# Optimization experiments

Measured on AMD Instinct MI355X. Metric: run time of the kernel, lower is better.

## Reference

```python
import jax, jax.numpy as jnp
import numpy as np

D_MODEL, D_FFN, N_LEVELS, N_HEADS, N_POINTS = 256, 1024, 4, 8, 4
B, LQ = 2, 8192
SHAPES = [(128, 128), (64, 64), (32, 32), (16, 16)]  # (H_l, W_l) per level
D_HEAD = D_MODEL // N_HEADS


def setup_inputs() -> dict:
    key = jax.random.key(0)
    ks = jax.random.split(key, 16)
    S = sum(h * w for h, w in SHAPES)

    def lin_w(k, fin, fout):
        s = 1.0 / np.sqrt(fin)
        return jax.random.uniform(k, (fin, fout), jnp.float32, -s, s)

    inp = {
        "tgt": jax.random.normal(ks[0], (B, LQ, D_MODEL), jnp.float32),
        "query_pos": jax.random.normal(ks[1], (B, LQ, D_MODEL), jnp.float32),
        "reference_points": jax.random.uniform(ks[2], (B, LQ, N_LEVELS, 2), jnp.float32),
        "src": jax.random.normal(ks[3], (B, S, D_MODEL), jnp.float32),
        "spatial_shapes": np.array(SHAPES, dtype=np.int64),
        "level_start_index": np.concatenate([[0], np.cumsum([h * w for h, w in SHAPES])[:-1]]).astype(np.int64),
        "W_value": lin_w(ks[4], D_MODEL, D_MODEL),
        "b_value": jnp.zeros((D_MODEL,), jnp.float32),
        "W_off": lin_w(ks[5], D_MODEL, N_HEADS * N_LEVELS * N_POINTS * 2),
        "b_off": 0.5 * jax.random.normal(ks[6], (N_HEADS * N_LEVELS * N_POINTS * 2,), jnp.float32),
        "W_attn": lin_w(ks[7], D_MODEL, N_HEADS * N_LEVELS * N_POINTS),
        "b_attn": jnp.zeros((N_HEADS * N_LEVELS * N_POINTS,), jnp.float32),
        "W_out": lin_w(ks[8], D_MODEL, D_MODEL),
        "b_out": jnp.zeros((D_MODEL,), jnp.float32),
        "ln1_g": jnp.ones((D_MODEL,), jnp.float32),
        "ln1_b": jnp.zeros((D_MODEL,), jnp.float32),
        "W1": lin_w(ks[9], D_MODEL, D_FFN),
        "b1": jnp.zeros((D_FFN,), jnp.float32),
        "W2": lin_w(ks[10], D_FFN, D_MODEL),
        "b2": jnp.zeros((D_MODEL,), jnp.float32),
        "ln3_g": jnp.ones((D_MODEL,), jnp.float32),
        "ln3_b": jnp.zeros((D_MODEL,), jnp.float32),
    }
    return inp


def _layer_norm(x, g, b, eps=1e-5):
    mu = jnp.mean(x, -1, keepdims=True)
    var = jnp.mean((x - mu) ** 2, -1, keepdims=True)
    return (x - mu) * jax.lax.rsqrt(var + eps) * g + b


def _ms_deform_attn(q, reference_points, src, shapes,
                    W_value, b_value, W_off, b_off, W_attn, b_attn, W_out, b_out):
    Bq, Lq, _ = q.shape
    value = (src @ W_value + b_value).reshape(Bq, -1, N_HEADS, D_HEAD)
    value = jnp.transpose(value, (0, 2, 1, 3))  # [B, H, S, Dh]
    off = (q @ W_off + b_off).reshape(Bq, Lq, N_HEADS, N_LEVELS, N_POINTS, 2)
    attn = jax.nn.softmax((q @ W_attn + b_attn).reshape(Bq, Lq, N_HEADS, N_LEVELS * N_POINTS), axis=-1)
    attn = attn.reshape(Bq, Lq, N_HEADS, N_LEVELS, N_POINTS)
    # offset normalizer is (W_l, H_l) per level
    normalizer = jnp.array([[w, h] for h, w in shapes], jnp.float32)
    loc = reference_points[:, :, None, :, None, :] + off / normalizer[None, None, None, :, None, :]

    out = jnp.zeros((Bq, Lq, N_HEADS, D_HEAD), jnp.float32)
    start = 0
    for l, (Hl, Wl) in enumerate(shapes):
        Nl = Hl * Wl
        v_l = value[:, :, start:start + Nl]  # [B, H, Nl, Dh]
        start += Nl
        loc_l = jnp.transpose(loc[:, :, :, l, :, :], (0, 2, 1, 3, 4))  # [B, H, Lq, P, 2]
        # grid_sample (align_corners=False, zero padding) pixel coords
        x = loc_l[..., 0] * Wl - 0.5
        y = loc_l[..., 1] * Hl - 0.5
        x0, y0 = jnp.floor(x), jnp.floor(y)
        wx, wy = x - x0, y - y0
        acc = jnp.zeros((Bq, N_HEADS, Lq, N_POINTS, D_HEAD), jnp.float32)
        for dx, dy, w in ((0, 0, (1 - wx) * (1 - wy)), (1, 0, wx * (1 - wy)),
                          (0, 1, (1 - wx) * wy), (1, 1, wx * wy)):
            xi, yi = x0 + dx, y0 + dy
            valid = (xi >= 0) & (xi < Wl) & (yi >= 0) & (yi < Hl)
            idx = (jnp.clip(yi, 0, Hl - 1) * Wl + jnp.clip(xi, 0, Wl - 1)).astype(jnp.int32)
            g = jnp.take_along_axis(v_l, idx.reshape(Bq, N_HEADS, -1, 1), axis=2)
            g = g.reshape(Bq, N_HEADS, Lq, N_POINTS, D_HEAD)
            acc = acc + jnp.where(valid[..., None], w[..., None] * g, 0.0)
        a = jnp.transpose(attn[:, :, :, l, :], (0, 2, 1, 3))  # [B, H, Lq, P]
        out = out + jnp.einsum('bhqp,bhqpd->bqhd', a, acc)
    return out.reshape(Bq, Lq, D_MODEL) @ W_out + b_out


def reference(tgt, query_pos, reference_points, src, spatial_shapes, level_start_index,
              W_value, b_value, W_off, b_off, W_attn, b_attn, W_out, b_out,
              ln1_g, ln1_b, W1, b1, W2, b2, ln3_g, ln3_b):
    shapes = [(int(h), int(w)) for h, w in np.asarray(spatial_shapes)]
    q = tgt + query_pos  # with_pos_embed
    tgt2 = _ms_deform_attn(q, reference_points, src, shapes,
                           W_value, b_value, W_off, b_off, W_attn, b_attn, W_out, b_out)
    x = _layer_norm(tgt + tgt2, ln1_g, ln1_b)  # dropout = identity (eval)
    ff = jax.nn.relu(x @ W1 + b1) @ W2 + b2
    return _layer_norm(x + ff, ln3_g, ln3_b)
```

## Files before the change

### kernel.cpp

```cpp
#include <hip/hip_runtime.h>
#include <hip/hip_bf16.h>
#include <math.h>

#define D_MODEL   256
#define D_FFN     1024
#define N_LEVELS  4
#define N_HEADS   8
#define N_POINTS  4
#define BATCH     2
#define LQ        8192
#define S_TOTAL   21760
#define M_Q       (BATCH*LQ)
#define M_V       (BATCH*S_TOTAL)
#define VTILES    (M_V/128)

typedef __attribute__((ext_vector_type(8))) short bf16x8;
typedef __attribute__((ext_vector_type(4))) float floatx4;

struct alignas(8)  bh4 { __hip_bfloat16 a, b, c, d; };
struct alignas(16) bh8 { __hip_bfloat16 v[8]; };

__device__ __forceinline__ void gld_lds16(const void* g, void* l) {
    __builtin_amdgcn_global_load_lds(
        (const __attribute__((address_space(1))) void*)g,
        (__attribute__((address_space(3))) void*)l, 16, 0, 0);
}

template<int BM, int BN, int K>
__device__ __forceinline__ void gemm_core(const __hip_bfloat16* __restrict__ A,
                                          const __hip_bfloat16* __restrict__ Bt,
                                          int row0, int nb0,
                                          short* As, short* Bs,
                                          floatx4 (&acc)[BM/64][BN/16])
{
    constexpr int NT  = BN / 16;
    constexpr int AF  = BM / 64;
    constexpr int BCH = BN / 64;
    constexpr int NIT = K / 32;

    const int tid  = threadIdx.x;
    const int w    = tid >> 6;
    const int lane = tid & 63;
    const int quad = lane >> 4;
    const int l15  = lane & 15;
    const size_t K2 = (size_t)K * 2;

    const char* gA[AF]; int lA[AF];
#pragma unroll
    for (int i = 0; i < AF; i++) {
        int o = (w * AF + i) * 1024 + lane * 16;
        gA[i] = (const char*)A + (size_t)(row0 + (o >> 6)) * K2 + (o & 63);
        lA[i] = (w * AF + i) * 512;
    }
    const char* gB[BCH]; int lB[BCH];
#pragma unroll
    for (int j = 0; j < BCH; j++) {
        int o = (w * BCH + j) * 1024 + lane * 16;
        gB[j] = (const char*)Bt + (size_t)(nb0 + (o >> 6)) * K2 + (o & 63);
        lB[j] = (w * BCH + j) * 512;
    }

#pragma unroll
    for (int i = 0; i < AF; i++)  gld_lds16(gA[i], &As[lA[i]]);
#pragma unroll
    for (int j = 0; j < BCH; j++) gld_lds16(gB[j], &Bs[lB[j]]);

#pragma unroll 8
    for (int it = 0; it < NIT; ++it) {
        __syncthreads();
        const int cb = it & 1;
        if (it + 1 < NIT) {
            const size_t kb = (size_t)(it + 1) * 64;
            const int nb = cb ^ 1;
#pragma unroll
            for (int i = 0; i < AF; i++)  gld_lds16(gA[i] + kb, &As[nb * BM * 32 + lA[i]]);
#pragma unroll
            for (int j = 0; j < BCH; j++) gld_lds16(gB[j] + kb, &Bs[nb * BN * 32 + lB[j]]);
        }
        const short* Ab = &As[cb * BM * 32];
        const short* Bb = &Bs[cb * BN * 32];
        bf16x8 af[AF];
#pragma unroll
        for (int mi = 0; mi < AF; mi++)
            af[mi] = *(const bf16x8*)&Ab[(w * (AF * 16) + mi * 16 + l15) * 32 + quad * 8];
#pragma unroll
        for (int ni = 0; ni < NT; ni++) {
            bf16x8 bfr = *(const bf16x8*)&Bb[(ni * 16 + l15) * 32 + quad * 8];
#pragma unroll
            for (int mi = 0; mi < AF; mi++)
                acc[mi][ni] = __builtin_amdgcn_mfma_f32_16x16x32_bf16(af[mi], bfr, acc[mi][ni], 0, 0, 0);
        }
    }
}

template<int BM, int BN, int K, int EPI>
__global__ __launch_bounds__(256)
void mfma_gemm(const __hip_bfloat16* __restrict__ A,
               const __hip_bfloat16* __restrict__ Bt,
               const float* __restrict__ bias,
               const float* __restrict__ resid,
               const float* __restrict__ lng, const float* __restrict__ lnb,
               float* __restrict__ outf, __hip_bfloat16* __restrict__ outb,
               int ldOut)
{
    constexpr int NT = BN / 16, AF = BM / 64;
    __shared__ alignas(16) short As[2 * BM * 32];
    __shared__ alignas(16) short Bs[2 * BN * 32];

    const int tid = threadIdx.x, w = tid >> 6, lane = tid & 63;
    const int quad = lane >> 4, l15 = lane & 15;
    const int row0 = blockIdx.x * BM, nb0 = blockIdx.y * BN;

    floatx4 acc[AF][NT];
#pragma unroll
    for (int mi = 0; mi < AF; mi++)
#pragma unroll
        for (int ni = 0; ni < NT; ni++) acc[mi][ni] = (floatx4){0.f, 0.f, 0.f, 0.f};

    gemm_core<BM, BN, K>(A, Bt, row0, nb0, As, Bs, acc);

    float bias_c[NT];
#pragma unroll
    for (int ni = 0; ni < NT; ni++) bias_c[ni] = bias[nb0 + ni * 16 + l15];

    if (EPI == 4) {
        float gv[NT], bv[NT];
#pragma unroll
        for (int ni = 0; ni < NT; ni++) { gv[ni] = lng[ni * 16 + l15]; bv[ni] = lnb[ni * 16 + l15]; }
#pragma unroll
        for (int mi = 0; mi < AF; mi++)
#pragma unroll
            for (int r = 0; r < 4; r++) {
                int row = row0 + w * (AF * 16) + mi * 16 + quad * 4 + r;
                size_t rb = (size_t)row * 256;
                float s = 0.f, sq = 0.f, vv[NT];
#pragma unroll
                for (int ni = 0; ni < NT; ni++) {
                    float v = acc[mi][ni][r] + bias_c[ni] + resid[rb + ni * 16 + l15];
                    vv[ni] = v; s += v; sq += v * v;
                }
#pragma unroll
                for (int msk = 1; msk <= 8; msk <<= 1) {
                    s += __shfl_xor(s, msk); sq += __shfl_xor(sq, msk);
                }
                float mean = s * (1.f / 256.f);
                float var  = sq * (1.f / 256.f) - mean * mean;
                float rstd = rsqrtf(var + 1e-5f);
#pragma unroll
                for (int ni = 0; ni < NT; ni++) {
                    float o = (vv[ni] - mean) * rstd * gv[ni] + bv[ni];
                    outf[rb + ni * 16 + l15] = o;
                    if (outb) outb[rb + ni * 16 + l15] = __float2bfloat16(o);
                }
            }
        return;
    }

#pragma unroll
    for (int mi = 0; mi < AF; mi++)
#pragma unroll
        for (int r = 0; r < 4; r++) {
            int row = row0 + w * (AF * 16) + mi * 16 + quad * 4 + r;
            size_t rb = (size_t)row * ldOut + nb0;
#pragma unroll
            for (int ni = 0; ni < NT; ni++) {
                float v = fmaxf(acc[mi][ni][r] + bias_c[ni], 0.f);
                outb[rb + ni * 16 + l15] = __float2bfloat16(v);
            }
        }
}

__global__ __launch_bounds__(256)
void mfma_gemm_vq(const __hip_bfloat16* __restrict__ srcb,
                  const __hip_bfloat16* __restrict__ Wvt,
                  const float* __restrict__ b_value,
                  __hip_bfloat16* __restrict__ valueb,
                  const __hip_bfloat16* __restrict__ qb,
                  const __hip_bfloat16* __restrict__ Woat,
                  const float* __restrict__ b_off, const float* __restrict__ b_attn,
                  float* __restrict__ offb, float* __restrict__ attnb)
{
    __shared__ alignas(16) short As[2 * 128 * 32];
    __shared__ alignas(16) short Bs[2 * 128 * 32];

    const bool isV = blockIdx.x < VTILES;
    if (isV && blockIdx.y == 2) return;

    const int tid = threadIdx.x, w = tid >> 6, lane = tid & 63;
    const int quad = lane >> 4, l15 = lane & 15;
    const int nb0 = blockIdx.y * 128;

    floatx4 acc[2][8];
#pragma unroll
    for (int mi = 0; mi < 2; mi++)
#pragma unroll
        for (int ni = 0; ni < 8; ni++) acc[mi][ni] = (floatx4){0.f, 0.f, 0.f, 0.f};

    if (isV) {
        const int row0 = blockIdx.x * 128;
        gemm_core<128, 128, 256>(srcb, Wvt, row0, nb0, As, Bs, acc);
        float bias_c[8];
#pragma unroll
        for (int ni = 0; ni < 8; ni++) bias_c[ni] = b_value[nb0 + ni * 16 + l15];
#pragma unroll
        for (int mi = 0; mi < 2; mi++)
#pragma unroll
            for (int r = 0; r < 4; r++) {
                int row = row0 + w * 32 + mi * 16 + quad * 4 + r;
                size_t rb = (size_t)row * 256 + nb0;
#pragma unroll
                for (int ni = 0; ni < 8; ni++)
                    valueb[rb + ni * 16 + l15] = __float2bfloat16(acc[mi][ni][r] + bias_c[ni]);
            }
        return;
    }

    const int row0 = (blockIdx.x - VTILES) * 128;
    gemm_core<128, 128, 256>(qb, Woat, row0, nb0, As, Bs, acc);

    if (blockIdx.y < 2) {
        float bias_c[8];
#pragma unroll
        for (int ni = 0; ni < 8; ni++) bias_c[ni] = b_off[nb0 + ni * 16 + l15];
#pragma unroll
        for (int mi = 0; mi < 2; mi++)
#pragma unroll
            for (int r = 0; r < 4; r++) {
                int row = row0 + w * 32 + mi * 16 + quad * 4 + r;
                size_t rb = (size_t)row * 256 + nb0;
#pragma unroll
                for (int ni = 0; ni < 8; ni++)
                    offb[rb + ni * 16 + l15] = acc[mi][ni][r] + bias_c[ni];
            }
    } else {
        float bias_c[8];
#pragma unroll
        for (int ni = 0; ni < 8; ni++) bias_c[ni] = b_attn[ni * 16 + l15];
#pragma unroll
        for (int mi = 0; mi < 2; mi++)
#pragma unroll
            for (int r = 0; r < 4; r++) {
                int row = row0 + w * 32 + mi * 16 + quad * 4 + r;
                size_t rb = (size_t)row * 128;
#pragma unroll
                for (int ni = 0; ni < 8; ni++) {
                    float v = acc[mi][ni][r] + bias_c[ni];
                    float m = v;
#pragma unroll
                    for (int msk = 1; msk <= 8; msk <<= 1) m = fmaxf(m, __shfl_xor(m, msk));
                    float e = __expf(v - m);
                    float ssum = e;
#pragma unroll
                    for (int msk = 1; msk <= 8; msk <<= 1) ssum += __shfl_xor(ssum, msk);
                    attnb[rb + ni * 16 + l15] = e / ssum;
                }
            }
    }
}

__global__ __launch_bounds__(256)
void prep_kernel(const float* w0, const float* w1, const float* w2,
                 const float* w3, const float* w4, const float* w5,
                 __hip_bfloat16* o0, __hip_bfloat16* o1, __hip_bfloat16* o2,
                 __hip_bfloat16* o3, __hip_bfloat16* o4, __hip_bfloat16* o5,
                 const float* src, __hip_bfloat16* srcb,
                 const float* tgt, const float* qpos, __hip_bfloat16* qb)
{
    const int bx = blockIdx.x;
    if (bx < 736) {
        int t = bx;
        const float* s; __hip_bfloat16* dst; int Kd, Nd, tl;
        if      (t < 64)  { s = w0; dst = o0; Kd = 256;  Nd = 256;  tl = t; }
        else if (t < 128) { s = w1; dst = o1; Kd = 256;  Nd = 256;  tl = t - 64; }
        else if (t < 160) { s = w2; dst = o2; Kd = 256;  Nd = 128;  tl = t - 128; }
        else if (t < 224) { s = w3; dst = o3; Kd = 256;  Nd = 256;  tl = t - 160; }
        else if (t < 480) { s = w4; dst = o4; Kd = 256;  Nd = 1024; tl = t - 224; }
        else              { s = w5; dst = o5; Kd = 1024; Nd = 256;  tl = t - 480; }
        int ntn = Nd >> 5;
        int kt = tl / ntn, nt = tl - kt * ntn;
        __shared__ float T[32][33];
        int tx = threadIdx.x & 31, ty = threadIdx.x >> 5;
#pragma unroll
        for (int i = 0; i < 4; i++) {
            int k = kt * 32 + ty + i * 8;
            T[tx][ty + i * 8] = s[(size_t)k * Nd + nt * 32 + tx];
        }
        __syncthreads();
#pragma unroll
        for (int i = 0; i < 4; i++) {
            int n = nt * 32 + ty + i * 8;
            dst[(size_t)n * Kd + kt * 32 + tx] = __float2bfloat16(T[ty + i * 8][tx]);
        }
    } else if (bx < 736 + 10880) {
        int i = (bx - 736) * 256 + threadIdx.x;
        float4 v = ((const float4*)src)[i];
        ((bh4*)srcb)[i] = { __float2bfloat16(v.x), __float2bfloat16(v.y),
                            __float2bfloat16(v.z), __float2bfloat16(v.w) };
    } else {
        int i = (bx - 736 - 10880) * 256 + threadIdx.x;
        float4 x = ((const float4*)tgt)[i];
        float4 y = ((const float4*)qpos)[i];
        ((bh4*)qb)[i] = { __float2bfloat16(x.x + y.x), __float2bfloat16(x.y + y.y),
                          __float2bfloat16(x.z + y.z), __float2bfloat16(x.w + y.w) };
    }
}

#define QB 8
__global__ __launch_bounds__(256)
void sample_kernel(const float* __restrict__ refp, const float* __restrict__ offb,
                   const float* __restrict__ attn,
                   const __hip_bfloat16* __restrict__ value,
                   __hip_bfloat16* __restrict__ tgt2)
{
    __shared__ int2 spk[64 * 65];

    const int q0  = blockIdx.x * QB;
    const int tid = threadIdx.x;

#pragma unroll
    for (int k = 0; k < 4; k++) {
        const int it = tid + k * 256;
        const int ql = it >> 7, h = (it >> 4) & 7, lp = it & 15;
        const int l = lp >> 2, p = lp & 3;
        const int q = q0 + ql, b = q >> 13;
        const int Wl = 128 >> l;
        const int LST = (l == 0) ? 0 : (l == 1) ? 16384 : (l == 2) ? 20480 : 21504;

        const float rx = refp[((size_t)q * N_LEVELS + l) * 2 + 0];
        const float ry = refp[((size_t)q * N_LEVELS + l) * 2 + 1];
        const float ox = offb[(size_t)q * 256 + h * 32 + l * 8 + p * 2 + 0];
        const float oy = offb[(size_t)q * 256 + h * 32 + l * 8 + p * 2 + 1];
        const float a  = attn[(size_t)q * 128 + h * 16 + lp];

        const float x = rx * Wl - 0.5f + ox;
        const float y = ry * Wl - 0.5f + oy;
        const float x0f = floorf(x), y0f = floorf(y);
        const float wx = x - x0f, wy = y - y0f;
        const int ix = (int)x0f, iy = (int)y0f;
        const int base = b * S_TOTAL + LST;
        const int g = ql * 8 + h;
        const float cw[4] = {(1.f - wx) * (1.f - wy) * a, wx * (1.f - wy) * a,
                             (1.f - wx) * wy * a,         wx * wy * a};
#pragma unroll
        for (int c = 0; c < 4; c++) {
            const int xi = ix + (c & 1), yi = iy + (c >> 1);
            const bool valid = ((unsigned)xi < (unsigned)Wl) && ((unsigned)yi < (unsigned)Wl);
            spk[(lp * 4 + c) * 65 + g] =
                make_int2(valid ? base + yi * Wl + xi : base,
                          __float_as_int(valid ? cw[c] : 0.f));
        }
    }
    __syncthreads();

    const int ql = tid >> 5, h = (tid >> 2) & 7, d4 = tid & 3;
    const int q = q0 + ql, g = ql * 8 + h;
    const int c0 = h * 32 + d4 * 8;
    const char* vb = (const char*)value + (size_t)c0 * 2;

    float ac[8] = {0.f, 0.f, 0.f, 0.f, 0.f, 0.f, 0.f, 0.f};
#pragma unroll
    for (int sc = 0; sc < 64; sc++) {
        int2 pk = spk[sc * 65 + g];
        float wv = __int_as_float(pk.y);
        uint4 rv = *(const uint4*)(vb + ((size_t)(unsigned)pk.x << 9));
        ac[0] += wv * __uint_as_float(rv.x << 16);
        ac[1] += wv * __uint_as_float(rv.x & 0xffff0000u);
        ac[2] += wv * __uint_as_float(rv.y << 16);
        ac[3] += wv * __uint_as_float(rv.y & 0xffff0000u);
        ac[4] += wv * __uint_as_float(rv.z << 16);
        ac[5] += wv * __uint_as_float(rv.z & 0xffff0000u);
        ac[6] += wv * __uint_as_float(rv.w << 16);
        ac[7] += wv * __uint_as_float(rv.w & 0xffff0000u);
    }
    bh8 o;
#pragma unroll
    for (int i = 0; i < 8; i++) o.v[i] = __float2bfloat16(ac[i]);
    *(bh8*)(tgt2 + (size_t)q * 256 + c0) = o;
}

extern "C" void kernel_launch(void* const* d_in, const int* in_sizes, int n_in,
                              void* d_out, int out_size, void* d_ws, size_t ws_size,
                              hipStream_t stream) {
    const float* tgt     = (const float*)d_in[0];
    const float* qpos    = (const float*)d_in[1];
    const float* refp    = (const float*)d_in[2];
    const float* src     = (const float*)d_in[3];
    const float* W_value = (const float*)d_in[6];
    const float* b_value = (const float*)d_in[7];
    const float* W_off   = (const float*)d_in[8];
    const float* b_off   = (const float*)d_in[9];
    const float* W_attn  = (const float*)d_in[10];
    const float* b_attn  = (const float*)d_in[11];
    const float* W_out   = (const float*)d_in[12];
    const float* b_out   = (const float*)d_in[13];
    const float* ln1_g   = (const float*)d_in[14];
    const float* ln1_b   = (const float*)d_in[15];
    const float* W1      = (const float*)d_in[16];
    const float* b1      = (const float*)d_in[17];
    const float* W2      = (const float*)d_in[18];
    const float* b2      = (const float*)d_in[19];
    const float* ln3_g   = (const float*)d_in[20];
    const float* ln3_b   = (const float*)d_in[21];
    float* out = (float*)d_out;

    char* p = (char*)d_ws;
    auto nxt = [&](size_t b) { char* r = p; p += (b + 255) & ~(size_t)255; return r; };
    __hip_bfloat16* Wvt    = (__hip_bfloat16*)nxt((size_t)256 * 256 * 2);
    __hip_bfloat16* Woat   = (__hip_bfloat16*)nxt((size_t)384 * 256 * 2);
    __hip_bfloat16* Woutt  = (__hip_bfloat16*)nxt((size_t)256 * 256 * 2);
    __hip_bfloat16* W1t    = (__hip_bfloat16*)nxt((size_t)1024 * 256 * 2);
    __hip_bfloat16* W2t    = (__hip_bfloat16*)nxt((size_t)256 * 1024 * 2);
    __hip_bfloat16* srcb   = (__hip_bfloat16*)nxt((size_t)M_V * 256 * 2);
    __hip_bfloat16* qb     = (__hip_bfloat16*)nxt((size_t)M_Q * 256 * 2);
    __hip_bfloat16* valueb = (__hip_bfloat16*)nxt((size_t)M_V * 256 * 2);
    float*          offb   = (float*)nxt((size_t)M_Q * 256 * 4);
    float*          attnb  = (float*)nxt((size_t)M_Q * 128 * 4);
    __hip_bfloat16* tgt2b  = (__hip_bfloat16*)nxt((size_t)M_Q * 256 * 2);
    float*          x      = (float*)nxt((size_t)M_Q * 256 * 4);
    __hip_bfloat16* xb     = (__hip_bfloat16*)nxt((size_t)M_Q * 256 * 2);
    __hip_bfloat16* hb     = (__hip_bfloat16*)nxt((size_t)M_Q * 1024 * 2);

    dim3 blk(256);

    prep_kernel<<<dim3(736 + 10880 + 4096), blk, 0, stream>>>(
        W_value, W_off, W_attn, W_out, W1, W2,
        Wvt, Woat, Woat + 256 * 256, Woutt, W1t, W2t,
        src, srcb, tgt, qpos, qb);

    mfma_gemm_vq<<<dim3(VTILES + M_Q / 128, 3), blk, 0, stream>>>(
        srcb, Wvt, b_value, valueb, qb, Woat, b_off, b_attn, offb, attnb);

    sample_kernel<<<dim3(M_Q / QB), blk, 0, stream>>>(refp, offb, attnb, valueb, tgt2b);

    mfma_gemm<64, 256, 256, 4><<<dim3(M_Q / 64, 1), blk, 0, stream>>>(
        tgt2b, Woutt, b_out, tgt, ln1_g, ln1_b, x, xb, 256);

    mfma_gemm<128, 128, 256, 2><<<dim3(M_Q / 128, 8), blk, 0, stream>>>(
        xb, W1t, b1, nullptr, nullptr, nullptr, nullptr, hb, 1024);

    mfma_gemm<64, 256, 1024, 4><<<dim3(M_Q / 64, 1), blk, 0, stream>>>(
        hb, W2t, b2, x, ln3_g, ln3_b, out, nullptr, 256);
}
```

Measured before the change: 306.8 us.

## Split GEMM epilogue LayerNorm into separate kernels, split-K FFN2, pack sample metadata

```diff
diff --git a/kernel.cpp b/kernel.cpp
--- a/kernel.cpp
+++ b/kernel.cpp
@@ -1,5 +1,6 @@
 #include <hip/hip_runtime.h>
 #include <hip/hip_bf16.h>
+#include <hip/hip_fp16.h>
 #include <math.h>
 
 #define D_MODEL   256
@@ -29,7 +30,7 @@
 template<int BM, int BN, int K>
 __device__ __forceinline__ void gemm_core(const __hip_bfloat16* __restrict__ A,
                                           const __hip_bfloat16* __restrict__ Bt,
-                                          int row0, int nb0,
+                                          int row0, int nb0, int lda, int ldb,
                                           short* As, short* Bs,
                                           floatx4 (&acc)[BM/64][BN/16])
 {
@@ -43,20 +44,20 @@
     const int lane = tid & 63;
     const int quad = lane >> 4;
     const int l15  = lane & 15;
-    const size_t K2 = (size_t)K * 2;
+    const size_t ldaB = (size_t)lda * 2, ldbB = (size_t)ldb * 2;
 
     const char* gA[AF]; int lA[AF];
 #pragma unroll
     for (int i = 0; i < AF; i++) {
         int o = (w * AF + i) * 1024 + lane * 16;
-        gA[i] = (const char*)A + (size_t)(row0 + (o >> 6)) * K2 + (o & 63);
+        gA[i] = (const char*)A + (size_t)(row0 + (o >> 6)) * ldaB + (o & 63);
         lA[i] = (w * AF + i) * 512;
     }
     const char* gB[BCH]; int lB[BCH];
 #pragma unroll
     for (int j = 0; j < BCH; j++) {
         int o = (w * BCH + j) * 1024 + lane * 16;
-        gB[j] = (const char*)Bt + (size_t)(nb0 + (o >> 6)) * K2 + (o & 63);
+        gB[j] = (const char*)Bt + (size_t)(nb0 + (o >> 6)) * ldbB + (o & 63);
         lB[j] = (w * BCH + j) * 512;
     }
 
@@ -98,10 +99,8 @@
 void mfma_gemm(const __hip_bfloat16* __restrict__ A,
                const __hip_bfloat16* __restrict__ Bt,
                const float* __restrict__ bias,
-               const float* __restrict__ resid,
-               const float* __restrict__ lng, const float* __restrict__ lnb,
                float* __restrict__ outf, __hip_bfloat16* __restrict__ outb,
-               int ldOut)
+               int lda, int ldb, int ldOut, long zStride)
 {
     constexpr int NT = BN / 16, AF = BM / 64;
     __shared__ alignas(16) short As[2 * BM * 32];
@@ -110,6 +109,7 @@
     const int tid = threadIdx.x, w = tid >> 6, lane = tid & 63;
     const int quad = lane >> 4, l15 = lane & 15;
     const int row0 = blockIdx.x * BM, nb0 = blockIdx.y * BN;
+    const int z = blockIdx.z;
 
     floatx4 acc[AF][NT];
 #pragma unroll
@@ -117,45 +117,14 @@
 #pragma unroll
         for (int ni = 0; ni < NT; ni++) acc[mi][ni] = (floatx4){0.f, 0.f, 0.f, 0.f};
 
-    gemm_core<BM, BN, K>(A, Bt, row0, nb0, As, Bs, acc);
+    gemm_core<BM, BN, K>(A + (size_t)z * K, Bt + (size_t)z * K,
+                         row0, nb0, lda, ldb, As, Bs, acc);
 
     float bias_c[NT];
 #pragma unroll
-    for (int ni = 0; ni < NT; ni++) bias_c[ni] = bias[nb0 + ni * 16 + l15];
-
-    if (EPI == 4) {
-        float gv[NT], bv[NT];
-#pragma unroll
-        for (int ni = 0; ni < NT; ni++) { gv[ni] = lng[ni * 16 + l15]; bv[ni] = lnb[ni * 16 + l15]; }
-#pragma unroll
-        for (int mi = 0; mi < AF; mi++)
-#pragma unroll
-            for (int r = 0; r < 4; r++) {
-                int row = row0 + w * (AF * 16) + mi * 16 + quad * 4 + r;
-                size_t rb = (size_t)row * 256;
-                float s = 0.f, sq = 0.f, vv[NT];
-#pragma unroll
-                for (int ni = 0; ni < NT; ni++) {
-                    float v = acc[mi][ni][r] + bias_c[ni] + resid[rb + ni * 16 + l15];
-                    vv[ni] = v; s += v; sq += v * v;
-                }
-#pragma unroll
-                for (int msk = 1; msk <= 8; msk <<= 1) {
-                    s += __shfl_xor(s, msk); sq += __shfl_xor(sq, msk);
-                }
-                float mean = s * (1.f / 256.f);
-                float var  = sq * (1.f / 256.f) - mean * mean;
-                float rstd = rsqrtf(var + 1e-5f);
-#pragma unroll
-                for (int ni = 0; ni < NT; ni++) {
-                    float o = (vv[ni] - mean) * rstd * gv[ni] + bv[ni];
-                    outf[rb + ni * 16 + l15] = o;
-                    if (outb) outb[rb + ni * 16 + l15] = __float2bfloat16(o);
-                }
-            }
-        return;
-    }
-
+    for (int ni = 0; ni < NT; ni++) bias_c[ni] = bias ? bias[nb0 + ni * 16 + l15] : 0.f;
+
+    float* of = outf + (size_t)z * zStride;
 #pragma unroll
     for (int mi = 0; mi < AF; mi++)
 #pragma unroll
@@ -164,8 +133,9 @@
             size_t rb = (size_t)row * ldOut + nb0;
 #pragma unroll
             for (int ni = 0; ni < NT; ni++) {
-                float v = fmaxf(acc[mi][ni][r] + bias_c[ni], 0.f);
-                outb[rb + ni * 16 + l15] = __float2bfloat16(v);
+                float v = acc[mi][ni][r] + bias_c[ni];
+                if (EPI == 2) outb[rb + ni * 16 + l15] = __float2bfloat16(fmaxf(v, 0.f));
+                else          of[rb + ni * 16 + l15] = v;
             }
         }
 }
@@ -198,7 +168,7 @@
 
     if (isV) {
         const int row0 = blockIdx.x * 128;
-        gemm_core<128, 128, 256>(srcb, Wvt, row0, nb0, As, Bs, acc);
+        gemm_core<128, 128, 256>(srcb, Wvt, row0, nb0, 256, 256, As, Bs, acc);
         float bias_c[8];
 #pragma unroll
         for (int ni = 0; ni < 8; ni++) bias_c[ni] = b_value[nb0 + ni * 16 + l15];
@@ -216,7 +186,7 @@
     }
 
     const int row0 = (blockIdx.x - VTILES) * 128;
-    gemm_core<128, 128, 256>(qb, Woat, row0, nb0, As, Bs, acc);
+    gemm_core<128, 128, 256>(qb, Woat, row0, nb0, 256, 256, As, Bs, acc);
 
     if (blockIdx.y < 2) {
         float bias_c[8];
@@ -256,6 +226,49 @@
                 }
             }
     }
+}
+
+__global__ __launch_bounds__(256)
+void ln_kernel(const float* __restrict__ in1, const float* __restrict__ in2,
+               const float* __restrict__ resid, const float* __restrict__ bias,
+               const float* __restrict__ g, const float* __restrict__ b,
+               float* __restrict__ outf, __hip_bfloat16* __restrict__ outb)
+{
+    const int row  = blockIdx.x * 4 + (threadIdx.x >> 6);
+    const int lane = threadIdx.x & 63;
+    const size_t rb = (size_t)row * 256 + lane * 4;
+
+    float4 v = *(const float4*)(resid + rb);
+    float4 a = *(const float4*)(in1 + rb);
+    v.x += a.x; v.y += a.y; v.z += a.z; v.w += a.w;
+    if (in2) {
+        float4 c = *(const float4*)(in2 + rb);
+        v.x += c.x; v.y += c.y; v.z += c.z; v.w += c.w;
+    }
+    if (bias) {
+        float4 c = *(const float4*)(bias + lane * 4);
+        v.x += c.x; v.y += c.y; v.z += c.z; v.w += c.w;
+    }
+    float s  = v.x + v.y + v.z + v.w;
+    float sq = v.x * v.x + v.y * v.y + v.z * v.z + v.w * v.w;
+#pragma unroll
+    for (int msk = 1; msk <= 32; msk <<= 1) {
+        s += __shfl_xor(s, msk); sq += __shfl_xor(sq, msk);
+    }
+    float mean = s * (1.f / 256.f);
+    float var  = sq * (1.f / 256.f) - mean * mean;
+    float rstd = rsqrtf(var + 1e-5f);
+    float4 gg = *(const float4*)(g + lane * 4);
+    float4 bb = *(const float4*)(b + lane * 4);
+    float4 o;
+    o.x = (v.x - mean) * rstd * gg.x + bb.x;
+    o.y = (v.y - mean) * rstd * gg.y + bb.y;
+    o.z = (v.z - mean) * rstd * gg.z + bb.z;
+    o.w = (v.w - mean) * rstd * gg.w + bb.w;
+    *(float4*)(outf + rb) = o;
+    if (outb)
+        *(bh4*)(outb + rb) = { __float2bfloat16(o.x), __float2bfloat16(o.y),
+                               __float2bfloat16(o.z), __float2bfloat16(o.w) };
 }
 
 __global__ __launch_bounds__(256)
@@ -312,7 +325,7 @@
                    const __hip_bfloat16* __restrict__ value,
                    __hip_bfloat16* __restrict__ tgt2)
 {
-    __shared__ int2 spk[64 * 65];
+    __shared__ unsigned spk[64 * 65];
 
     const int q0  = blockIdx.x * QB;
     const int tid = threadIdx.x;
@@ -345,9 +358,9 @@
         for (int c = 0; c < 4; c++) {
             const int xi = ix + (c & 1), yi = iy + (c >> 1);
             const bool valid = ((unsigned)xi < (unsigned)Wl) && ((unsigned)yi < (unsigned)Wl);
-            spk[(lp * 4 + c) * 65 + g] =
-                make_int2(valid ? base + yi * Wl + xi : base,
-                          __float_as_int(valid ? cw[c] : 0.f));
+            const unsigned pix = valid ? (unsigned)(base + yi * Wl + xi) : (unsigned)base;
+            const __half hw = __float2half(valid ? cw[c] : 0.f);
+            spk[(lp * 4 + c) * 65 + g] = (pix << 16) | (unsigned)__half_as_ushort(hw);
         }
     }
     __syncthreads();
@@ -360,9 +373,9 @@
     float ac[8] = {0.f, 0.f, 0.f, 0.f, 0.f, 0.f, 0.f, 0.f};
 #pragma unroll
     for (int sc = 0; sc < 64; sc++) {
-        int2 pk = spk[sc * 65 + g];
-        float wv = __int_as_float(pk.y);
-        uint4 rv = *(const uint4*)(vb + ((size_t)(unsigned)pk.x << 9));
+        unsigned u = spk[sc * 65 + g];
+        float wv = __half2float(__ushort_as_half((unsigned short)(u & 0xffffu)));
+        uint4 rv = *(const uint4*)(vb + ((size_t)(u >> 16) << 9));
         ac[0] += wv * __uint_as_float(rv.x << 16);
         ac[1] += wv * __uint_as_float(rv.x & 0xffff0000u);
         ac[2] += wv * __uint_as_float(rv.y << 16);
@@ -419,6 +432,9 @@
     float*          x      = (float*)nxt((size_t)M_Q * 256 * 4);
     __hip_bfloat16* xb     = (__hip_bfloat16*)nxt((size_t)M_Q * 256 * 2);
     __hip_bfloat16* hb     = (__hip_bfloat16*)nxt((size_t)M_Q * 1024 * 2);
+    float* t2o = offb;
+    float* p0  = (float*)srcb;
+    float* p1  = p0 + (size_t)M_Q * 256;
 
     dim3 blk(256);
 
@@ -432,12 +448,18 @@
 
     sample_kernel<<<dim3(M_Q / QB), blk, 0, stream>>>(refp, offb, attnb, valueb, tgt2b);
 
-    mfma_gemm<64, 256, 256, 4><<<dim3(M_Q / 64, 1), blk, 0, stream>>>(
-        tgt2b, Woutt, b_out, tgt, ln1_g, ln1_b, x, xb, 256);
+    mfma_gemm<64, 128, 256, 0><<<dim3(M_Q / 64, 2), blk, 0, stream>>>(
+        tgt2b, Woutt, b_out, t2o, nullptr, 256, 256, 256, 0);
+
+    ln_kernel<<<dim3(M_Q / 4), blk, 0, stream>>>(
+        t2o, nullptr, tgt, nullptr, ln1_g, ln1_b, x, xb);
 
     mfma_gemm<128, 128, 256, 2><<<dim3(M_Q / 128, 8), blk, 0, stream>>>(
-        xb, W1t, b1, nullptr, nullptr, nullptr, nullptr, hb, 1024);
-
-    mfma_gemm<64, 256, 1024, 4><<<dim3(M_Q / 64, 1), blk, 0, stream>>>(
-        hb, W2t, b2, x, ln3_g, ln3_b, out, nullptr, 256);
-}
+        xb, W1t, b1, nullptr, hb, 256, 256, 1024, 0);
+
+    mfma_gemm<64, 128, 512, 0><<<dim3(M_Q / 64, 2, 2), blk, 0, stream>>>(
+        hb, W2t, nullptr, p0, nullptr, 1024, 1024, 256, (long)M_Q * 256);
+
+    ln_kernel<<<dim3(M_Q / 4), blk, 0, stream>>>(
+        p0, p1, x, b2, ln3_g, ln3_b, out, nullptr);
+}
```

Measured after the change: 301.2 us. Within noise of the previous version (-1.8%).
